# Kernel optimization log

Hardware: AMD Instinct MI355X
Metric: run time of the kernel (lower is better)

Reference implementation:

```python
import jax, jax.numpy as jnp
import numpy as np
import math

N, E, IN, C, H, ED, B = 50000, 800000, 64, 32, 4, 1, 64
HC = H * C
EPS = 1e-5


def setup_inputs() -> dict:
    key = jax.random.key(0)
    ks = jax.random.split(key, 16)
    def lin(k, fan_in, fan_out):
        s = 1.0 / math.sqrt(fan_in)
        return jax.random.normal(k, (fan_in, fan_out), jnp.float32) * s
    inp = {
        "x": jax.random.normal(ks[0], (N, IN), jnp.float32),
        "edge_index": jax.random.randint(ks[1], (2, E), 0, N, jnp.int64),
        "edge_attr": jax.random.normal(ks[2], (E, ED), jnp.float32),
        "batch_index": jnp.sort(jax.random.randint(ks[3], (N,), 0, B, jnp.int64)),
        # TransformerConv params
        "Wq": lin(ks[4], IN, HC), "bq": jnp.zeros((HC,), jnp.float32),
        "Wk": lin(ks[5], IN, HC), "bk": jnp.zeros((HC,), jnp.float32),
        "Wv": lin(ks[6], IN, HC), "bv": jnp.zeros((HC,), jnp.float32),
        "We": lin(ks[7], ED, HC), "be": jnp.zeros((HC,), jnp.float32),
        "Wskip": lin(ks[8], IN, HC), "bskip": jnp.zeros((HC,), jnp.float32),
        "Wbeta": lin(ks[9], 3 * HC, 1),
        # post linear: H*C -> C
        "Wlin": lin(ks[10], HC, C), "blin": jnp.zeros((C,), jnp.float32),
        # GraphNorm params
        "gn_weight": jnp.ones((C,), jnp.float32),
        "gn_bias": jnp.zeros((C,), jnp.float32),
        "gn_mean_scale": jnp.ones((C,), jnp.float32),
    }
    return inp


def reference(x, edge_index, edge_attr, batch_index, Wq, bq, Wk, bk, Wv, bv,
              We, be, Wskip, bskip, Wbeta, Wlin, blin,
              gn_weight, gn_bias, gn_mean_scale):
    src, dst = edge_index[0], edge_index[1]
    # dense projections [N, H, C]
    q = (x @ Wq + bq).reshape(N, H, C)
    k = (x @ Wk + bk).reshape(N, H, C)
    v = (x @ Wv + bv).reshape(N, H, C)
    e = (edge_attr @ We + be).reshape(E, H, C)
    # per-edge attention logits [E, H]
    k_e = k[src] + e
    alpha = jnp.einsum('ehc,ehc->eh', q[dst], k_e) / math.sqrt(C)
    # segment softmax over incoming edges of each dst node
    m = jax.ops.segment_max(alpha, dst, num_segments=N)  # [N, H]
    a = jnp.exp(alpha - m[dst])
    denom = jax.ops.segment_sum(a, dst, num_segments=N)  # [N, H]
    a = a / jnp.maximum(denom, 1e-16)[dst]
    # (dropout p=0.3 on attention is a no-op in eval mode)
    msg = (v[src] + e) * a[:, :, None]                    # [E, H, C]
    out = jax.ops.segment_sum(msg, dst, num_segments=N).reshape(N, HC)
    # beta-gated skip connection
    x_r = x @ Wskip + bskip                               # [N, HC]
    beta = jax.nn.sigmoid(jnp.concatenate([out, x_r, out - x_r], -1) @ Wbeta)
    out = beta * x_r + (1.0 - beta) * out
    # linear + relu
    h = jax.nn.relu(out @ Wlin + blin)                    # [N, C]
    # GraphNorm over per-graph segments
    ones = jnp.ones((N, 1), h.dtype)
    cnt = jax.ops.segment_sum(ones, batch_index, num_segments=B)  # [B, 1]
    cnt = jnp.maximum(cnt, 1.0)
    mean = jax.ops.segment_sum(h, batch_index, num_segments=B) / cnt
    centered = h - mean[batch_index] * gn_mean_scale
    var = jax.ops.segment_sum(centered * centered, batch_index, num_segments=B) / cnt
    std = jnp.sqrt(var + EPS)
    return gn_weight * centered / std[batch_index] + gn_bias
```

## Files before the change

### kernel.cpp

```cpp
#include <hip/hip_runtime.h>
#include <math.h>

static constexpr int kN  = 50000;
static constexpr int kE  = 800000;
static constexpr int kC  = 32;
static constexpr int kH  = 4;
static constexpr int kHC = 128;
static constexpr int kB  = 64;
static constexpr int kNB = (kN + 255) / 256;
static constexpr int kMB = (kN + 127) / 128;

typedef __attribute__((ext_vector_type(8))) short bf16x8;
typedef __attribute__((ext_vector_type(4))) float f32x4;

__device__ __forceinline__ unsigned short f2bf(float f) {
    unsigned u = __float_as_uint(f);
    unsigned r = (u + 0x7FFFu + ((u >> 16) & 1u)) >> 16;
    return (unsigned short)r;
}
__device__ __forceinline__ float blo(unsigned u) { return __uint_as_float(u << 16); }
__device__ __forceinline__ float bhi(unsigned u) { return __uint_as_float(u & 0xFFFF0000u); }

__global__ __launch_bounds__(256) void hist_packw_kernel(
    const int* __restrict__ ei, int* __restrict__ deg,
    const float* __restrict__ Wq, const float* __restrict__ Wk,
    const float* __restrict__ Wv, const float* __restrict__ Wskip,
    uint4* __restrict__ wtf)
{
    if (blockIdx.x < 16) {
        int tid = blockIdx.x * 256 + threadIdx.x;
        int f = tid >> 6, l = tid & 63;
        int m = f >> 4, c = (f >> 1) & 7, kk = f & 1;
        int col = c * 16 + (l & 15);
        int k0  = kk * 32 + (l >> 4) * 8;
        const float* Wm = (m == 0) ? Wq : (m == 1) ? Wk : (m == 2) ? Wv : Wskip;
        unsigned p[4];
#pragma unroll
        for (int j = 0; j < 4; ++j) {
            unsigned lo = f2bf(Wm[(k0 + 2 * j) * kHC + col]);
            unsigned hi = f2bf(Wm[(k0 + 2 * j + 1) * kHC + col]);
            p[j] = lo | (hi << 16);
        }
        wtf[f * 64 + l] = make_uint4(p[0], p[1], p[2], p[3]);
        return;
    }
    int i = (blockIdx.x - 16) * 256 + threadIdx.x;
    if (i < kE) atomicAdd(&deg[ei[kE + i]], 1);
}

__global__ __launch_bounds__(256) void proj_scanA_kernel(
    const float4* __restrict__ x4,
    const float* __restrict__ bq, const float* __restrict__ bk,
    const float* __restrict__ bv, const float* __restrict__ bskip,
    const uint4* __restrict__ wtf,
    unsigned short* __restrict__ qxb, unsigned short* __restrict__ kvb,
    const int* __restrict__ deg, int* __restrict__ bsum)
{
    __shared__ int sh4[4];
    if (blockIdx.x >= kMB) {
        int bid = blockIdx.x - kMB;
        int i = bid * 256 + threadIdx.x;
        int v = (i < kN) ? deg[i] : 0;
#pragma unroll
        for (int s = 1; s < 64; s <<= 1) v += __shfl_xor(v, s);
        if ((threadIdx.x & 63) == 0) sh4[threadIdx.x >> 6] = v;
        __syncthreads();
        if (threadIdx.x == 0) bsum[bid] = sh4[0] + sh4[1] + sh4[2] + sh4[3];
        return;
    }
    const int t = threadIdx.x;
    const int w = t >> 6;
    const int l = t & 63;
    const int l15 = l & 15, l16 = l >> 4;
    const int n0 = blockIdx.x * 128;

    bf16x8 bf[8][2];
#pragma unroll
    for (int c = 0; c < 8; ++c)
#pragma unroll
        for (int kk = 0; kk < 2; ++kk)
            bf[c][kk] = __builtin_bit_cast(bf16x8, wtf[(unsigned)((w * 16 + c * 2 + kk) * 64 + l)]);

    const float* Bm = (w == 0) ? bq : (w == 1) ? bk : (w == 2) ? bv : bskip;
    float bias[8];
#pragma unroll
    for (int c = 0; c < 8; ++c) bias[c] = Bm[c * 16 + l15];

    unsigned short* dst = (w == 0 || w == 3) ? qxb : kvb;
    const int add4 = (w >= 2) ? 4 : 0;

    for (int rt = 0; rt < 4; ++rt) {
        const int r0 = n0 + rt * 32 + l15;
        const int r1 = r0 + 16;
        f32x4 acc[2][8];
#pragma unroll
        for (int r = 0; r < 2; ++r)
#pragma unroll
            for (int c = 0; c < 8; ++c)
                acc[r][c] = (f32x4){bias[c], bias[c], bias[c], bias[c]};
#pragma unroll
        for (int kk = 0; kk < 2; ++kk) {
            float4 xa0 = make_float4(0.f,0.f,0.f,0.f), xb0 = xa0, xa1 = xa0, xb1 = xa0;
            if (r0 < kN) {
                xa0 = x4[(size_t)r0 * 16 + kk * 8 + l16 * 2];
                xb0 = x4[(size_t)r0 * 16 + kk * 8 + l16 * 2 + 1];
            }
            if (r1 < kN) {
                xa1 = x4[(size_t)r1 * 16 + kk * 8 + l16 * 2];
                xb1 = x4[(size_t)r1 * 16 + kk * 8 + l16 * 2 + 1];
            }
            uint4 u0 = make_uint4(
                f2bf(xa0.x) | ((unsigned)f2bf(xa0.y) << 16),
                f2bf(xa0.z) | ((unsigned)f2bf(xa0.w) << 16),
                f2bf(xb0.x) | ((unsigned)f2bf(xb0.y) << 16),
                f2bf(xb0.z) | ((unsigned)f2bf(xb0.w) << 16));
            uint4 u1 = make_uint4(
                f2bf(xa1.x) | ((unsigned)f2bf(xa1.y) << 16),
                f2bf(xa1.z) | ((unsigned)f2bf(xa1.w) << 16),
                f2bf(xb1.x) | ((unsigned)f2bf(xb1.y) << 16),
                f2bf(xb1.z) | ((unsigned)f2bf(xb1.w) << 16));
            bf16x8 a0 = __builtin_bit_cast(bf16x8, u0);
            bf16x8 a1 = __builtin_bit_cast(bf16x8, u1);
#pragma unroll
            for (int c = 0; c < 8; ++c) {
                acc[0][c] = __builtin_amdgcn_mfma_f32_16x16x32_bf16(a0, bf[c][kk], acc[0][c], 0, 0, 0);
                acc[1][c] = __builtin_amdgcn_mfma_f32_16x16x32_bf16(a1, bf[c][kk], acc[1][c], 0, 0, 0);
            }
        }
#pragma unroll
        for (int r = 0; r < 2; ++r) {
#pragma unroll
            for (int j = 0; j < 4; ++j) {
                int node = n0 + rt * 32 + r * 16 + l16 * 4 + j;
                bool valid = (node < kN) && ((l & 1) == 0);
                size_t base = (size_t)node * 128;
#pragma unroll
                for (int c = 0; c < 8; ++c) {
                    float v0 = acc[r][c][j];
                    float v1 = __shfl_xor(v0, 1);
                    if (valid) {
                        int jcol = c * 16 + l15;
                        int gpos = ((jcol >> 2) << 3) | (jcol & 3);
                        unsigned pk = f2bf(v0) | ((unsigned)f2bf(v1) << 16);
                        ((unsigned*)dst)[base + ((gpos + add4) >> 1)] = pk;
                    }
                }
            }
        }
    }
}

__global__ __launch_bounds__(256) void scanC2_kernel(
    const int* __restrict__ deg, const int* __restrict__ bsum,
    int* __restrict__ rowptr, int* __restrict__ cursor)
{
    __shared__ int bsh[256];
    __shared__ int sh[256];
    const int t = threadIdx.x, i = blockIdx.x * 256 + t;
    int bv = (t < kNB) ? bsum[t] : 0;
    bsh[t] = bv; __syncthreads();
    for (int off = 1; off < 256; off <<= 1) {
        int u = (t >= off) ? bsh[t - off] : 0;
        __syncthreads();
        bsh[t] += u;
        __syncthreads();
    }
    const int bofs = (blockIdx.x == 0) ? 0 : bsh[blockIdx.x - 1];
    if (blockIdx.x == 0 && t == 0) rowptr[kN] = bsh[kNB - 1];
    int v = (i < kN) ? deg[i] : 0;
    sh[t] = v; __syncthreads();
    for (int off = 1; off < 256; off <<= 1) {
        int u = (t >= off) ? sh[t - off] : 0;
        __syncthreads();
        sh[t] += u;
        __syncthreads();
    }
    if (i < kN) {
        int ex = sh[t] - v + bofs;
        rowptr[i] = ex;
        cursor[i] = ex;
    }
}

__global__ __launch_bounds__(256) void scatter_kernel(
    const int* __restrict__ ei, const float* __restrict__ ea,
    int* __restrict__ cursor, int2* __restrict__ csr)
{
    int i = blockIdx.x * 256 + threadIdx.x;
    if (i >= kE) return;
    int dst = ei[kE + i];
    int slot = atomicAdd(&cursor[dst], 1);
    csr[slot] = make_int2(ei[i], __float_as_int(ea[i]));
}

__global__ __launch_bounds__(256) void node_attn_kernel(
    const int* __restrict__ rowptr, const int2* __restrict__ csr,
    const unsigned short* __restrict__ qxb, const unsigned short* __restrict__ kvb,
    const float* __restrict__ We, const float* __restrict__ be,
    const float* __restrict__ Wbeta, const float* __restrict__ Wlin,
    const float* __restrict__ blin, float* __restrict__ hbuf)
{
    __shared__ float wlS[kHC * kC];
    __shared__ float wbS[3 * kHC];
    __shared__ float oshS[4][kHC];
    const int t = threadIdx.x, wv = t >> 6, lane = t & 63;
    for (int i = t; i < kHC * kC; i += 256) wlS[i] = Wlin[i];
    for (int i = t; i < 3 * kHC; i += 256) wbS[i] = Wbeta[i];
    __syncthreads();

    const int node = blockIdx.x * 4 + wv;
    const int half = lane >> 5;
    const int sl   = lane & 31;
    const int ch   = sl * 4;
    const float4 we4 = *(const float4*)&We[ch];
    const float4 be4 = *(const float4*)&be[ch];
    const float4 wbA = *(const float4*)&wbS[ch];
    const float4 wbB = *(const float4*)&wbS[kHC + ch];
    const float4 wbC = *(const float4*)&wbS[2 * kHC + ch];
    const float blc = blin[sl];
    const float A2 = 0.17677669529663687f * 1.44269504088896341f;

    const uint4 qx = *((const uint4*)(qxb + (size_t)node * 256) + sl);
    const float q0 = blo(qx.x), q1 = bhi(qx.x), q2v = blo(qx.y), q3 = bhi(qx.y);
    const float xr0 = blo(qx.z), xr1 = bhi(qx.z), xr2 = blo(qx.w), xr3 = bhi(qx.w);
    float qw = q0 * we4.x + q1 * we4.y + q2v * we4.z + q3 * we4.w;
    float qe = q0 * be4.x + q1 * be4.y + q2v * be4.z + q3 * be4.w;
    qw += __shfl_xor(qw, 1); qe += __shfl_xor(qe, 1);
    qw += __shfl_xor(qw, 2); qe += __shfl_xor(qe, 2);
    qw += __shfl_xor(qw, 4); qe += __shfl_xor(qe, 4);
    const float qwA = qw * A2, qbA = qe * A2;

    float ss = 0.f, swa = 0.f;
    float ax0 = 0.f, ax1 = 0.f, ax2 = 0.f, ax3 = 0.f;
    const int beg = rowptr[node], end = rowptr[node + 1];
    int e = beg;
    for (; e + 3 < end; e += 4) {
        int2 cA = csr[e + half];
        int2 cB = csr[e + 2 + half];
        const uint4 uA = *((const uint4*)(kvb + (size_t)cA.x * 256) + sl);
        const uint4 uB = *((const uint4*)(kvb + (size_t)cB.x * 256) + sl);
        float aA = __int_as_float(cA.y), aB = __int_as_float(cB.y);
        float pA = fmaf(q3, bhi(uA.y), fmaf(q2v, blo(uA.y), fmaf(q1, bhi(uA.x), q0 * blo(uA.x))));
        float pB = fmaf(q3, bhi(uB.y), fmaf(q2v, blo(uB.y), fmaf(q1, bhi(uB.x), q0 * blo(uB.x))));
        pA += __shfl_xor(pA, 1); pB += __shfl_xor(pB, 1);
        pA += __shfl_xor(pA, 2); pB += __shfl_xor(pB, 2);
        pA += __shfl_xor(pA, 4); pB += __shfl_xor(pB, 4);
        float eA = __builtin_amdgcn_exp2f(fmaf(pA, A2, fmaf(aA, qwA, qbA)));
        float eB = __builtin_amdgcn_exp2f(fmaf(pB, A2, fmaf(aB, qwA, qbA)));
        ss  += eA + eB;
        swa = fmaf(eA, aA, fmaf(eB, aB, swa));
        ax0 = fmaf(eA, blo(uA.z), fmaf(eB, blo(uB.z), ax0));
        ax1 = fmaf(eA, bhi(uA.z), fmaf(eB, bhi(uB.z), ax1));
        ax2 = fmaf(eA, blo(uA.w), fmaf(eB, blo(uB.w), ax2));
        ax3 = fmaf(eA, bhi(uA.w), fmaf(eB, bhi(uB.w), ax3));
    }
    for (; e < end; e += 2) {
        int idx = e + half;
        bool valid = idx < end;
        int2 cA = csr[valid ? idx : end - 1];
        const uint4 uA = *((const uint4*)(kvb + (size_t)cA.x * 256) + sl);
        float aA = __int_as_float(cA.y);
        float pA = fmaf(q3, bhi(uA.y), fmaf(q2v, blo(uA.y), fmaf(q1, bhi(uA.x), q0 * blo(uA.x))));
        pA += __shfl_xor(pA, 1);
        pA += __shfl_xor(pA, 2);
        pA += __shfl_xor(pA, 4);
        float eA = valid ? __builtin_amdgcn_exp2f(fmaf(pA, A2, fmaf(aA, qwA, qbA))) : 0.f;
        ss  += eA;
        swa = fmaf(eA, aA, swa);
        ax0 = fmaf(eA, blo(uA.z), ax0);
        ax1 = fmaf(eA, bhi(uA.z), ax1);
        ax2 = fmaf(eA, blo(uA.w), ax2);
        ax3 = fmaf(eA, bhi(uA.w), ax3);
    }
    ss  += __shfl_xor(ss , 32);
    swa += __shfl_xor(swa, 32);
    ax0 += __shfl_xor(ax0, 32);
    ax1 += __shfl_xor(ax1, 32);
    ax2 += __shfl_xor(ax2, 32);
    ax3 += __shfl_xor(ax3, 32);

    float rcp = 1.f / fmaxf(ss, 1e-16f);
    float v0 = fmaf(swa, we4.x, fmaf(ss, be4.x, ax0)) * rcp;
    float v1 = fmaf(swa, we4.y, fmaf(ss, be4.y, ax1)) * rcp;
    float v2 = fmaf(swa, we4.z, fmaf(ss, be4.z, ax2)) * rcp;
    float v3 = fmaf(swa, we4.w, fmaf(ss, be4.w, ax3)) * rcp;
    float part = wbA.x * v0 + wbA.y * v1 + wbA.z * v2 + wbA.w * v3
               + wbB.x * xr0 + wbB.y * xr1 + wbB.z * xr2 + wbB.w * xr3
               + wbC.x * (v0 - xr0) + wbC.y * (v1 - xr1)
               + wbC.z * (v2 - xr2) + wbC.w * (v3 - xr3);
    part += __shfl_xor(part, 1);
    part += __shfl_xor(part, 2);
    part += __shfl_xor(part, 4);
    part += __shfl_xor(part, 8);
    part += __shfl_xor(part, 16);
    float beta = 1.f / (1.f + __expf(-part));
    float o0 = beta * xr0 + (1.f - beta) * v0;
    float o1 = beta * xr1 + (1.f - beta) * v1;
    float o2 = beta * xr2 + (1.f - beta) * v2;
    float o3 = beta * xr3 + (1.f - beta) * v3;
    if (half == 0) *(float4*)&oshS[wv][ch] = make_float4(o0, o1, o2, o3);
    __builtin_amdgcn_wave_barrier();
    float hp = 0.f;
#pragma unroll
    for (int jj = 0; jj < 64; ++jj) {
        int j = half * 64 + jj;
        hp = fmaf(oshS[wv][j], wlS[j * kC + sl], hp);
    }
    hp += __shfl_xor(hp, 32);
    if (lane < 32) hbuf[(size_t)node * kC + sl] = fmaxf(hp + blc, 0.f);
}

__global__ __launch_bounds__(256) void gn_reduce_kernel(
    const float* __restrict__ hbuf, const int* __restrict__ batch,
    const float* __restrict__ gms, float* __restrict__ stats)
{
    const int g = blockIdx.x;
    const int t = threadIdx.x;
    __shared__ int se[2];
    __shared__ float s1[8][kC], s2[8][kC];
    if (t < 2) {
        int target = g + t;
        int lo = 0, hi = kN;
        while (lo < hi) { int mid = (lo + hi) >> 1; if (batch[mid] < target) lo = mid + 1; else hi = mid; }
        se[t] = lo;
    }
    __syncthreads();
    int start = se[0], end = se[1];
    float cnt = fmaxf((float)(end - start), 1.f);
    int c = t & 31, r = t >> 5;
    float a = 0.f, b = 0.f;
    for (int n = start + r; n < end; n += 8) {
        float v = hbuf[(size_t)n * kC + c];
        a += v; b = fmaf(v, v, b);
    }
    s1[r][c] = a; s2[r][c] = b;
    __syncthreads();
    if (t < kC) {
        float sa = 0.f, sb = 0.f;
#pragma unroll
        for (int i = 0; i < 8; ++i) { sa += s1[i][t]; sb += s2[i][t]; }
        float mean = sa / cnt;
        float ms   = mean * gms[t];
        float var  = sb / cnt - 2.f * ms * mean + ms * ms;
        stats[g * 64 + t]      = ms;
        stats[g * 64 + 32 + t] = rsqrtf(var + 1e-5f);
    }
}

__global__ __launch_bounds__(256) void gn_apply_kernel(
    const float* __restrict__ hbuf, const int* __restrict__ batch,
    const float* __restrict__ stats,
    const float* __restrict__ gw, const float* __restrict__ gb,
    float* __restrict__ out)
{
    int idx = blockIdx.x * 256 + threadIdx.x;
    if (idx >= kN * kC) return;
    int n = idx >> 5, c = idx & 31;
    int g = batch[n];
    float ms   = stats[g * 64 + c];
    float rstd = stats[g * 64 + 32 + c];
    float v = hbuf[idx];
    out[idx] = fmaf(gw[c] * (v - ms), rstd, gb[c]);
}

extern "C" void kernel_launch(void* const* d_in, const int* in_sizes, int n_in,
                              void* d_out, int out_size, void* d_ws, size_t ws_size,
                              hipStream_t stream) {
    (void)in_sizes; (void)n_in; (void)out_size; (void)ws_size;
    const float* x     = (const float*)d_in[0];
    const int*   ei    = (const int*)d_in[1];
    const float* ea    = (const float*)d_in[2];
    const int*   batch = (const int*)d_in[3];
    const float* Wq    = (const float*)d_in[4];
    const float* bq    = (const float*)d_in[5];
    const float* Wk    = (const float*)d_in[6];
    const float* bk    = (const float*)d_in[7];
    const float* Wv    = (const float*)d_in[8];
    const float* bv    = (const float*)d_in[9];
    const float* We    = (const float*)d_in[10];
    const float* be    = (const float*)d_in[11];
    const float* Wskip = (const float*)d_in[12];
    const float* bskip = (const float*)d_in[13];
    const float* Wbeta = (const float*)d_in[14];
    const float* Wlin  = (const float*)d_in[15];
    const float* blin  = (const float*)d_in[16];
    const float* gw    = (const float*)d_in[17];
    const float* gb    = (const float*)d_in[18];
    const float* gms   = (const float*)d_in[19];
    float* out = (float*)d_out;

    char* ws = (char*)d_ws;
    int2*  csr    = (int2*)ws;            ws += (size_t)kE * 8;
    unsigned short* qxb = (unsigned short*)ws; ws += (size_t)kN * 256 * 2;
    unsigned short* kvb = (unsigned short*)ws; ws += (size_t)kN * 256 * 2;
    float* hbuf   = (float*)ws;           ws += (size_t)kN * kC * 4;
    int*   deg    = (int*)ws;             ws += (size_t)kN * 4;
    int*   cursor = (int*)ws;             ws += (size_t)kN * 4;
    int*   rowptr = (int*)ws;             ws += (size_t)(kN + 1) * 4;
    int*   bsum   = (int*)ws;             ws += (size_t)kNB * 4;
    float* stats  = (float*)ws;           ws += (size_t)kB * 64 * 4;
    uint4* wtf    = (uint4*)ws;           ws += (size_t)64 * 64 * 16;

    hipMemsetAsync(deg, 0, (size_t)kN * 4, stream);

    hist_packw_kernel<<<16 + (kE + 255) / 256, 256, 0, stream>>>(
        ei, deg, Wq, Wk, Wv, Wskip, wtf);
    proj_scanA_kernel<<<kMB + kNB, 256, 0, stream>>>(
        (const float4*)x, bq, bk, bv, bskip, wtf, qxb, kvb, deg, bsum);
    scanC2_kernel<<<kNB, 256, 0, stream>>>(deg, bsum, rowptr, cursor);
    scatter_kernel<<<(kE + 255) / 256, 256, 0, stream>>>(ei, ea, cursor, csr);
    node_attn_kernel<<<kN / 4, 256, 0, stream>>>(
        rowptr, csr, qxb, kvb, We, be, Wbeta, Wlin, blin, hbuf);
    gn_reduce_kernel<<<kB, 256, 0, stream>>>(hbuf, batch, gms, stats);
    gn_apply_kernel<<<(kN * kC + 255) / 256, 256, 0, stream>>>(
        hbuf, batch, stats, gw, gb, out);
}
```

Before: 233.1 us.

## Stage projection stores through LDS and pack CSR entries into 32 bits

The projection kernel now writes its bf16 results into a shared-memory staging buffer, then stores them to the q/skip and k/v buffers as coalesced 16-byte row writes instead of scattered 4-byte stores. Each CSR entry shrinks from 8 to 4 bytes: a 16-bit source index plus the edge attribute rounded to bf16. This halves CSR write and gather traffic in the scatter and attention kernels. The attention kernel also moves from 256 to 512 threads per block, 8 nodes each. In exchange, the 32 KB of staging LDS and extra barriers may lower projection occupancy, the edge attribute loses precision, and the 16-bit index only works while N stays below 65536.

Result: slower. 238.7 us (+2.4%).

```diff
diff --git a/kernel.cpp b/kernel.cpp
--- a/kernel.cpp
+++ b/kernel.cpp
@@ -56,16 +56,17 @@
     unsigned short* __restrict__ qxb, unsigned short* __restrict__ kvb,
     const int* __restrict__ deg, int* __restrict__ bsum)
 {
-    __shared__ int sh4[4];
+    __shared__ unsigned stg[2][32 * 128];
     if (blockIdx.x >= kMB) {
         int bid = blockIdx.x - kMB;
         int i = bid * 256 + threadIdx.x;
         int v = (i < kN) ? deg[i] : 0;
 #pragma unroll
         for (int s = 1; s < 64; s <<= 1) v += __shfl_xor(v, s);
-        if ((threadIdx.x & 63) == 0) sh4[threadIdx.x >> 6] = v;
-        __syncthreads();
-        if (threadIdx.x == 0) bsum[bid] = sh4[0] + sh4[1] + sh4[2] + sh4[3];
+        if ((threadIdx.x & 63) == 0) stg[0][threadIdx.x >> 6] = (unsigned)v;
+        __syncthreads();
+        if (threadIdx.x == 0)
+            bsum[bid] = (int)(stg[0][0] + stg[0][1] + stg[0][2] + stg[0][3]);
         return;
     }
     const int t = threadIdx.x;
@@ -86,8 +87,8 @@
 #pragma unroll
     for (int c = 0; c < 8; ++c) bias[c] = Bm[c * 16 + l15];
 
-    unsigned short* dst = (w == 0 || w == 3) ? qxb : kvb;
-    const int add4 = (w >= 2) ? 4 : 0;
+    const int bufid = (w == 0 || w == 3) ? 0 : 1;
+    const int add4  = (w >= 2) ? 4 : 0;
 
     for (int rt = 0; rt < 4; ++rt) {
         const int r0 = n0 + rt * 32 + l15;
@@ -131,22 +132,34 @@
         for (int r = 0; r < 2; ++r) {
 #pragma unroll
             for (int j = 0; j < 4; ++j) {
-                int node = n0 + rt * 32 + r * 16 + l16 * 4 + j;
-                bool valid = (node < kN) && ((l & 1) == 0);
-                size_t base = (size_t)node * 128;
+                int nn = r * 16 + l16 * 4 + j;
 #pragma unroll
                 for (int c = 0; c < 8; ++c) {
                     float v0 = acc[r][c][j];
                     float v1 = __shfl_xor(v0, 1);
-                    if (valid) {
+                    if ((l & 1) == 0) {
                         int jcol = c * 16 + l15;
                         int gpos = ((jcol >> 2) << 3) | (jcol & 3);
-                        unsigned pk = f2bf(v0) | ((unsigned)f2bf(v1) << 16);
-                        ((unsigned*)dst)[base + ((gpos + add4) >> 1)] = pk;
+                        stg[bufid][nn * 128 + ((gpos + add4) >> 1)] =
+                            f2bf(v0) | ((unsigned)f2bf(v1) << 16);
                     }
                 }
             }
         }
+        __syncthreads();
+#pragma unroll
+        for (int i = 0; i < 8; ++i) {
+            int idx = i * 256 + t;
+            int buf = idx >> 10;
+            int rem = idx & 1023;
+            int nn  = rem >> 5;
+            int q4  = rem & 31;
+            int node = n0 + rt * 32 + nn;
+            if (node < kN)
+                ((uint4*)(buf ? kvb : qxb))[(size_t)node * 32 + q4] =
+                    *(const uint4*)&stg[buf][nn * 128 + q4 * 4];
+        }
+        __syncthreads();
     }
 }
 
@@ -184,17 +197,17 @@
 
 __global__ __launch_bounds__(256) void scatter_kernel(
     const int* __restrict__ ei, const float* __restrict__ ea,
-    int* __restrict__ cursor, int2* __restrict__ csr)
+    int* __restrict__ cursor, unsigned* __restrict__ csr)
 {
     int i = blockIdx.x * 256 + threadIdx.x;
     if (i >= kE) return;
     int dst = ei[kE + i];
     int slot = atomicAdd(&cursor[dst], 1);
-    csr[slot] = make_int2(ei[i], __float_as_int(ea[i]));
-}
-
-__global__ __launch_bounds__(256) void node_attn_kernel(
-    const int* __restrict__ rowptr, const int2* __restrict__ csr,
+    csr[slot] = (unsigned)ei[i] | ((unsigned)f2bf(ea[i]) << 16);
+}
+
+__global__ __launch_bounds__(512) void node_attn_kernel(
+    const int* __restrict__ rowptr, const unsigned* __restrict__ csr,
     const unsigned short* __restrict__ qxb, const unsigned short* __restrict__ kvb,
     const float* __restrict__ We, const float* __restrict__ be,
     const float* __restrict__ Wbeta, const float* __restrict__ Wlin,
@@ -202,13 +215,13 @@
 {
     __shared__ float wlS[kHC * kC];
     __shared__ float wbS[3 * kHC];
-    __shared__ float oshS[4][kHC];
+    __shared__ float oshS[8][kHC];
     const int t = threadIdx.x, wv = t >> 6, lane = t & 63;
-    for (int i = t; i < kHC * kC; i += 256) wlS[i] = Wlin[i];
-    for (int i = t; i < 3 * kHC; i += 256) wbS[i] = Wbeta[i];
+    for (int i = t; i < kHC * kC; i += 512) wlS[i] = Wlin[i];
+    for (int i = t; i < 3 * kHC; i += 512) wbS[i] = Wbeta[i];
     __syncthreads();
 
-    const int node = blockIdx.x * 4 + wv;
+    const int node = blockIdx.x * 8 + wv;
     const int half = lane >> 5;
     const int sl   = lane & 31;
     const int ch   = sl * 4;
@@ -235,11 +248,11 @@
     const int beg = rowptr[node], end = rowptr[node + 1];
     int e = beg;
     for (; e + 3 < end; e += 4) {
-        int2 cA = csr[e + half];
-        int2 cB = csr[e + 2 + half];
-        const uint4 uA = *((const uint4*)(kvb + (size_t)cA.x * 256) + sl);
-        const uint4 uB = *((const uint4*)(kvb + (size_t)cB.x * 256) + sl);
-        float aA = __int_as_float(cA.y), aB = __int_as_float(cB.y);
+        unsigned cA = csr[e + half];
+        unsigned cB = csr[e + 2 + half];
+        float aA = bhi(cA), aB = bhi(cB);
+        const uint4 uA = *((const uint4*)(kvb + (size_t)(cA & 0xFFFFu) * 256) + sl);
+        const uint4 uB = *((const uint4*)(kvb + (size_t)(cB & 0xFFFFu) * 256) + sl);
         float pA = fmaf(q3, bhi(uA.y), fmaf(q2v, blo(uA.y), fmaf(q1, bhi(uA.x), q0 * blo(uA.x))));
         float pB = fmaf(q3, bhi(uB.y), fmaf(q2v, blo(uB.y), fmaf(q1, bhi(uB.x), q0 * blo(uB.x))));
         pA += __shfl_xor(pA, 1); pB += __shfl_xor(pB, 1);
@@ -257,9 +270,9 @@
     for (; e < end; e += 2) {
         int idx = e + half;
         bool valid = idx < end;
-        int2 cA = csr[valid ? idx : end - 1];
-        const uint4 uA = *((const uint4*)(kvb + (size_t)cA.x * 256) + sl);
-        float aA = __int_as_float(cA.y);
+        unsigned cA = csr[valid ? idx : end - 1];
+        float aA = bhi(cA);
+        const uint4 uA = *((const uint4*)(kvb + (size_t)(cA & 0xFFFFu) * 256) + sl);
         float pA = fmaf(q3, bhi(uA.y), fmaf(q2v, blo(uA.y), fmaf(q1, bhi(uA.x), q0 * blo(uA.x))));
         pA += __shfl_xor(pA, 1);
         pA += __shfl_xor(pA, 2);
@@ -390,7 +403,7 @@
     float* out = (float*)d_out;
 
     char* ws = (char*)d_ws;
-    int2*  csr    = (int2*)ws;            ws += (size_t)kE * 8;
+    unsigned* csr = (unsigned*)ws;        ws += (size_t)kE * 4;
     unsigned short* qxb = (unsigned short*)ws; ws += (size_t)kN * 256 * 2;
     unsigned short* kvb = (unsigned short*)ws; ws += (size_t)kN * 256 * 2;
     float* hbuf   = (float*)ws;           ws += (size_t)kN * kC * 4;
@@ -409,7 +422,7 @@
         (const float4*)x, bq, bk, bv, bskip, wtf, qxb, kvb, deg, bsum);
     scanC2_kernel<<<kNB, 256, 0, stream>>>(deg, bsum, rowptr, cursor);
     scatter_kernel<<<(kE + 255) / 256, 256, 0, stream>>>(ei, ea, cursor, csr);
-    node_attn_kernel<<<kN / 4, 256, 0, stream>>>(
+    node_attn_kernel<<<kN / 8, 512, 0, stream>>>(
         rowptr, csr, qxb, kvb, We, be, Wbeta, Wlin, blin, hbuf);
     gn_reduce_kernel<<<kB, 256, 0, stream>>>(hbuf, batch, gms, stats);
     gn_apply_kernel<<<(kN * kC + 255) / 256, 256, 0, stream>>>(
```
